# Kernel optimization log

Measured on AMD Instinct MI355X. Metric: run time of the kernel, lower is better.

Reference implementation:

```python
import jax, jax.numpy as jnp
import numpy as np

B, S = 256, 512
NQ = 1000           # n_skills
MEM, DK, DV, FC = 20, 50, 200, 50  # memory_size, key dim, value dim, final fc dim


def _kaiming(key, shape, fan_in):
    return jax.random.normal(key, shape) * np.float32(np.sqrt(2.0 / fan_in))


def setup_inputs() -> dict:
    key = jax.random.key(0)
    ks = jax.random.split(key, 12)
    q_data = jax.random.randint(ks[0], (B, S), 0, NQ + 1)
    qa_data = jax.random.randint(ks[1], (B, S), 0, 2 * NQ + 1)
    u = jax.random.uniform(ks[2], (B * S,))
    # target: -1 = masked/padding, else binary label (matches target.ge(0) masking)
    target = jnp.where(u < 0.1, -1.0, (u > 0.55).astype(jnp.float32))
    q_embed_w = _kaiming(ks[3], (NQ + 1, DK), DK)
    qa_embed_w = _kaiming(ks[4], (2 * NQ + 1, DV), DV)
    memory_key = _kaiming(ks[5], (MEM, DK), DK)
    init_memory_value = _kaiming(ks[6], (MEM, DV), DV)
    erase_w = _kaiming(ks[7], (DV, DV), DV)
    erase_b = jnp.zeros((DV,), jnp.float32)
    add_w = _kaiming(ks[8], (DV, DV), DV)
    add_b = jnp.zeros((DV,), jnp.float32)
    read_w = _kaiming(ks[9], (DV + FC, FC), DV + FC)
    read_b = jnp.zeros((FC,), jnp.float32)
    pred_w = _kaiming(ks[10], (FC, 1), FC)
    pred_b = jnp.zeros((1,), jnp.float32)
    return dict(q_data=q_data, qa_data=qa_data, target=target,
                q_embed_w=q_embed_w, qa_embed_w=qa_embed_w,
                memory_key=memory_key, init_memory_value=init_memory_value,
                erase_w=erase_w, erase_b=erase_b, add_w=add_w, add_b=add_b,
                read_w=read_w, read_b=read_b, pred_w=pred_w, pred_b=pred_b)


def reference(q_data, qa_data, target, q_embed_w, qa_embed_w, memory_key,
              init_memory_value, erase_w, erase_b, add_w, add_b,
              read_w, read_b, pred_w, pred_b):
    b = q_data.shape[0]
    q_e = q_embed_w[q_data]     # [B,S,DK]
    qa_e = qa_embed_w[qa_data]  # [B,S,DV]
    Mv0 = jnp.broadcast_to(init_memory_value, (b, MEM, DV))

    def step(Mv, xs):
        q_t, qa_t = xs                                        # [B,DK], [B,DV]
        corr = jax.nn.softmax(q_t @ memory_key.T, axis=1)     # [B,MEM] addressing
        read = jnp.einsum('bm,bmd->bd', corr, Mv)             # weighted read
        erase = jax.nn.sigmoid(qa_t @ erase_w + erase_b)      # [B,DV]
        add = jnp.tanh(qa_t @ add_w + add_b)                  # [B,DV]
        w = corr[:, :, None]                                  # [B,MEM,1]
        Mv = Mv * (1.0 - w * erase[:, None, :]) + w * add[:, None, :]
        return Mv, read

    _, reads = jax.lax.scan(step, Mv0, (q_e.transpose(1, 0, 2), qa_e.transpose(1, 0, 2)))
    reads = reads.transpose(1, 0, 2)                          # [B,S,DV]
    x = jnp.concatenate([reads, q_e], axis=-1)                # [B,S,DV+FC]
    h = jnp.tanh(x @ read_w + read_b)                         # [B,S,FC]
    logits = (h @ pred_w + pred_b).reshape(-1)                # [B*S]
    mask = target >= 0.0
    t = jnp.where(mask, target, 0.0)
    # numerically-stable BCE-with-logits, masked mean
    bce = jnp.maximum(logits, 0.0) - logits * t + jnp.log1p(jnp.exp(-jnp.abs(logits)))
    loss = jnp.sum(jnp.where(mask, bce, 0.0)) / jnp.maximum(mask.sum(), 1)
    return loss, jax.nn.sigmoid(logits)
```

## Files before the change

kernel.cpp:

```cpp
#include <hip/hip_runtime.h>
#include <math.h>

#define B_   256
#define S_   512
#define NQ_  1000
#define MEM_ 20
#define DK_  50
#define DV_  200
#define FC_  50
#define RPB  4
#define CHK  16
#define CLEN (S_/CHK)
#define NKS  7
#define XS_STRIDE 232
#define CORR_STRIDE 12
#define NB_EA    ((2*NQ_+1+RPB-1)/RPB)
#define NB_CORR  4
#define NB_WPACK 7
#define NB_HQ    251
#define PREP1_BLOCKS (NB_EA+NB_CORR)
#define MM_BLOCKS (B_*CHK)
#define SCANA_BLOCKS (B_*(CHK-1))
#define SCANA_TOTAL (SCANA_BLOCKS+NB_WPACK+NB_HQ)

typedef __attribute__((ext_vector_type(8))) short bf16x8_t;
typedef __attribute__((ext_vector_type(4))) float f32x4_t;
typedef __attribute__((ext_vector_type(2))) _Float16 f16x2_t;

static __device__ __forceinline__ f16x2_t h2(unsigned u){ return __builtin_bit_cast(f16x2_t, u); }
static __device__ __forceinline__ unsigned h2u(f16x2_t v){ return __builtin_bit_cast(unsigned, v); }
static __device__ __forceinline__ unsigned packh2(float x, float y){
  unsigned short bx = __builtin_bit_cast(unsigned short, (_Float16)x);
  unsigned short by = __builtin_bit_cast(unsigned short, (_Float16)y);
  return (unsigned)bx | ((unsigned)by << 16);
}
static __device__ __forceinline__ f16x2_t pkfma16(f16x2_t a, f16x2_t b, f16x2_t c){
  return __builtin_elementwise_fma(a, b, c);
}

static __device__ __forceinline__ unsigned short f2bf(float f){
  unsigned u = __float_as_uint(f);
  unsigned r = u + 0x7fffu + ((u >> 16) & 1u);
  return (unsigned short)(r >> 16);
}
static __device__ __forceinline__ float ftanh(float x){
  float e = __expf(2.f*x);
  return 1.f - 2.f*__builtin_amdgcn_rcpf(e+1.f);
}
static __device__ __forceinline__ float fsigm(float x){
  return __builtin_amdgcn_rcpf(1.f+__expf(-x));
}

__global__ __launch_bounds__(256) void k_prep1(
    const float* __restrict__ qaw,
    const float* __restrict__ ew, const float* __restrict__ eb,
    const float* __restrict__ aw, const float* __restrict__ ab,
    uint2* __restrict__ eaTab,
    const float* __restrict__ qw, const float* __restrict__ mk,
    unsigned* __restrict__ corrH){
  __shared__ float qa[RPB*DV_];
  int blk = blockIdx.x;
  if(blk < NB_EA){
    int row0 = blk*RPB;
    for(int i=threadIdx.x; i<RPB*DV_; i+=256){
      int r = i/DV_, cc = i - r*DV_;
      int row = row0 + r;
      qa[i] = (row <= 2*NQ_) ? qaw[row*DV_+cc] : 0.f;
    }
    __syncthreads();
    int d = threadIdx.x;
    if(d >= DV_) return;
    float accE[RPB], accA[RPB];
    #pragma unroll
    for(int r=0;r<RPB;++r){ accE[r] = eb[d]; accA[r] = ab[d]; }
    float we0 = ew[d], wa0 = aw[d];
    for(int j=0;j<DV_;++j){
      int jn = (j+1 < DV_) ? j+1 : j;
      float we1 = ew[jn*DV_+d];
      float wa1 = aw[jn*DV_+d];
      #pragma unroll
      for(int r=0;r<RPB;++r){
        float x = qa[r*DV_+j];
        accE[r] = fmaf(x, we0, accE[r]);
        accA[r] = fmaf(x, wa0, accA[r]);
      }
      we0 = we1; wa0 = wa1;
    }
    #pragma unroll
    for(int r=0;r<RPB;++r){
      int row = row0 + r;
      if(row <= 2*NQ_){
        unsigned he = (unsigned)__builtin_bit_cast(unsigned short, (_Float16)fsigm(accE[r]));
        unsigned ha = (unsigned)__builtin_bit_cast(unsigned short, (_Float16)ftanh(accA[r]));
        eaTab[(size_t)row*DV_+d] = make_uint2(he*0x10001u, ha*0x10001u);
      }
    }
  } else {
    int q = (blk-NB_EA)*256 + threadIdx.x;
    if(q > NQ_) return;
    float qv[DK_];
    #pragma unroll
    for(int j=0;j<DK_;++j) qv[j] = qw[q*DK_+j];
    float s[MEM_]; float mx = -1e30f;
    #pragma unroll
    for(int m=0;m<MEM_;++m){
      float acc = 0.f;
      #pragma unroll
      for(int j=0;j<DK_;++j) acc = fmaf(qv[j], mk[m*DK_+j], acc);
      s[m] = acc; mx = fmaxf(mx, acc);
    }
    float sum = 0.f;
    #pragma unroll
    for(int m=0;m<MEM_;++m){ s[m] = __expf(s[m]-mx); sum += s[m]; }
    float inv = __builtin_amdgcn_rcpf(sum);
    #pragma unroll
    for(int i=0;i<MEM_/2;++i)
      corrH[q*CORR_STRIDE+i] = packh2(s[2*i]*inv, s[2*i+1]*inv);
  }
}

__global__ __launch_bounds__(256,8) void k_scanA(const int* __restrict__ qd,
    const int* __restrict__ qad,
    const unsigned* __restrict__ corrH,
    const uint2* __restrict__ eaTab,
    unsigned* __restrict__ ABu,
    const float* __restrict__ qw,
    const float* __restrict__ rw, const float* __restrict__ rb,
    const float* __restrict__ pw,
    unsigned short* __restrict__ WpFrag, float* __restrict__ pwPad,
    float* __restrict__ hq){
  const int blk = blockIdx.x;
  if(blk >= SCANA_BLOCKS){
    int xblk = blk - SCANA_BLOCKS;
    if(xblk < NB_WPACK){
      int ks = xblk;
      int nt = threadIdx.x >> 6;
      int lane = threadIdx.x & 63;
      int quad = lane >> 4, col = lane & 15;
      int n = nt*16 + col;
      unsigned short tmp[8];
      #pragma unroll
      for(int j=0;j<8;++j){
        int k = ks*32 + quad*8 + j;
        tmp[j] = (k < DV_ && n < FC_) ? f2bf(rw[k*FC_+n]) : (unsigned short)0;
      }
      uint4* dst = reinterpret_cast<uint4*>(WpFrag + ((size_t)(ks*4+nt)*64 + lane)*8);
      *dst = *reinterpret_cast<const uint4*>(tmp);
      if(ks == 0 && threadIdx.x < 64)
        pwPad[threadIdx.x] = (threadIdx.x < FC_) ? pw[threadIdx.x] : 0.f;
    } else {
      int idx = (xblk-NB_WPACK)*256 + threadIdx.x;
      int q = idx >> 6, n = idx & 63;
      if(q > NQ_) return;
      float v = 0.f;
      if(n < FC_){
        float acc = rb[n];
        #pragma unroll
        for(int j=0;j<DK_;++j)
          acc = fmaf(qw[q*DK_+j], rw[(DV_+j)*FC_+n], acc);
        v = acc;
      }
      hq[q*64+n] = v;
    }
    return;
  }

  const int b = blk / (CHK-1), c = blk % (CHK-1);
  const int d = threadIdx.x;
  const int dc = (d < DV_) ? d : DV_-1;
  const bool act = (d < DV_);
  const int* __restrict__ qp  = qd  + b*S_ + c*CLEN;
  const int* __restrict__ qap = qad + b*S_ + c*CLEN;

  const f16x2_t one2h = {(_Float16)1.f, (_Float16)1.f};
  f16x2_t A2[MEM_/2], B2[MEM_/2];
  #pragma unroll
  for(int i=0;i<MEM_/2;++i){ A2[i] = one2h; B2[i] = (f16x2_t){(_Float16)0.f,(_Float16)0.f}; }

  int q2   = qp[1];
  int qaT2 = qap[2];
  int qaT3 = qap[3];
  int q1s  = __builtin_amdgcn_readfirstlane(qp[0]);
  const unsigned* cp0 = corrH + q1s*CORR_STRIDE;
  uint4 ca = *(const uint4*)(cp0);
  uint4 cb = *(const uint4*)(cp0+4);
  uint2 cc = *(const uint2*)(cp0+8);
  uint2 ea  = eaTab[(size_t)qap[0]*DV_ + dc];
  uint2 ean = eaTab[(size_t)qap[1]*DV_ + dc];

  #pragma unroll 4
  for(int t=0;t<CLEN;++t){
    int t2 = (t+2 < CLEN) ? t+2 : CLEN-1;
    int t4 = (t+4 < CLEN) ? t+4 : CLEN-1;
    int q3 = qp[t2];
    int qaN = qap[t4];
    int qs = __builtin_amdgcn_readfirstlane(q2);
    const unsigned* cpn_ = corrH + qs*CORR_STRIDE;
    uint4 na = *(const uint4*)(cpn_);
    uint4 nb = *(const uint4*)(cpn_+4);
    uint2 nc = *(const uint2*)(cpn_+8);
    uint2 eann = eaTab[(size_t)qaT2*DV_ + dc];

    const f16x2_t ee = h2(ea.x), aa = h2(ea.y);
    #define UPDA(u, i) { \
      f16x2_t cp = h2(u); \
      f16x2_t al = pkfma16(-cp, ee, one2h); \
      f16x2_t be = cp*aa; \
      A2[i] = A2[i]*al; \
      B2[i] = pkfma16(al, B2[i], be); }
    UPDA(ca.x, 0)  UPDA(ca.y, 1)  UPDA(ca.z, 2)  UPDA(ca.w, 3)
    UPDA(cb.x, 4)  UPDA(cb.y, 5)  UPDA(cb.z, 6)  UPDA(cb.w, 7)
    UPDA(cc.x, 8)  UPDA(cc.y, 9)
    #undef UPDA

    ca=na; cb=nb; cc=nc;
    ea=ean; ean=eann;
    q2=q3; qaT2=qaT3; qaT3=qaN;
  }
  if(act){
    unsigned* base = ABu + ((size_t)(b*(CHK-1) + c)*MEM_)*DV_ + d;
    #pragma unroll
    for(int i=0;i<MEM_/2;++i){
      unsigned a01 = h2u(A2[i]);
      unsigned b01 = h2u(B2[i]);
      base[(size_t)(2*i)*DV_]   = (a01 & 0xffffu) | (b01 << 16);
      base[(size_t)(2*i+1)*DV_] = (a01 >> 16)     | (b01 & 0xffff0000u);
    }
  }
}

__global__ __launch_bounds__(256) void k_prefix(const float* __restrict__ mv0,
    const unsigned* __restrict__ ABu, unsigned* __restrict__ Mv0p){
  int i = blockIdx.x*256 + threadIdx.x;
  if(i >= B_*(MEM_/2)*DV_) return;
  int d = i % DV_;
  int p = (i / DV_) % (MEM_/2);
  int b = i / (DV_*(MEM_/2));
  float MvE = mv0[(2*p)*DV_+d];
  float MvO = mv0[(2*p+1)*DV_+d];
  #pragma unroll
  for(int c=1;c<CHK;++c){
    unsigned vE = ABu[((size_t)(b*(CHK-1) + (c-1))*MEM_ + 2*p)*DV_ + d];
    unsigned vO = ABu[((size_t)(b*(CHK-1) + (c-1))*MEM_ + 2*p+1)*DV_ + d];
    MvE = fmaf((float)h2(vE)[0], MvE, (float)h2(vE)[1]);
    MvO = fmaf((float)h2(vO)[0], MvO, (float)h2(vO)[1]);
    Mv0p[((size_t)(b*CHK + c)*(MEM_/2) + p)*DV_ + d] = packh2(MvE, MvO);
  }
}

__global__ __launch_bounds__(256,8) void k_scan_mm(const int* __restrict__ qd,
    const int* __restrict__ qad,
    const unsigned* __restrict__ corrH,
    const uint2* __restrict__ eaTab,
    const float* __restrict__ mv0,
    const unsigned* __restrict__ Mv0p,
    const unsigned short* __restrict__ WpFrag,
    const float* __restrict__ hq,
    const float* __restrict__ pwPad, const float* __restrict__ pb,
    const float* __restrict__ target,
    float* __restrict__ out, float2* __restrict__ partials){
  __shared__ unsigned short Xs[CLEN*XS_STRIDE];
  __shared__ float sred[2][2][16];
  __shared__ float sbce[4];

  const int blk = blockIdx.x;
  const int b = blk >> 4, c = blk & (CHK-1);
  const int d = threadIdx.x;
  const int dc = (d < DV_) ? d : DV_-1;
  const bool act = (d < DV_);
  const bool padw = (d < 224);
  const int* __restrict__ qp  = qd  + b*S_ + c*CLEN;
  const int* __restrict__ qap = qad + b*S_ + c*CLEN;

  const int wave = threadIdx.x >> 6;
  const int lane = threadIdx.x & 63;
  const int col  = lane & 15, quad = lane >> 4;
  const int rt   = wave & 1;
  const int nh   = wave >> 1;
  const int mbase = rt*16;

  int qpre[4];
  #pragma unroll
  for(int reg=0;reg<4;++reg) qpre[reg] = qp[mbase + quad*4 + reg];

  f16x2_t Mv2[MEM_/2];
  if(c == 0){
    #pragma unroll
    for(int i=0;i<MEM_/2;++i)
      Mv2[i] = (f16x2_t){ (_Float16)mv0[(2*i)*DV_+dc], (_Float16)mv0[(2*i+1)*DV_+dc] };
  } else {
    const unsigned* base = Mv0p + ((size_t)(b*CHK + c)*(MEM_/2))*DV_ + dc;
    #pragma unroll
    for(int i=0;i<MEM_/2;++i)
      Mv2[i] = h2(base[(size_t)i*DV_]);
  }

  int q2   = qp[1];
  int qaT2 = qap[2];
  int qaT3 = qap[3];
  int q1s  = __builtin_amdgcn_readfirstlane(qp[0]);
  const unsigned* cp0 = corrH + q1s*CORR_STRIDE;
  uint4 ca = *(const uint4*)(cp0);
  uint4 cb = *(const uint4*)(cp0+4);
  uint2 cc = *(const uint2*)(cp0+8);
  uint2 ea  = eaTab[(size_t)qap[0]*DV_ + dc];
  uint2 ean = eaTab[(size_t)qap[1]*DV_ + dc];

  #pragma unroll 4
  for(int t=0;t<CLEN;++t){
    int t2 = (t+2 < CLEN) ? t+2 : CLEN-1;
    int t4 = (t+4 < CLEN) ? t+4 : CLEN-1;
    int q3 = qp[t2];
    int qaN = qap[t4];
    int qs = __builtin_amdgcn_readfirstlane(q2);
    const unsigned* cpn_ = corrH + qs*CORR_STRIDE;
    uint4 na = *(const uint4*)(cpn_);
    uint4 nb = *(const uint4*)(cpn_+4);
    uint2 nc = *(const uint2*)(cpn_+8);
    uint2 eann = eaTab[(size_t)qaT2*DV_ + dc];

    const f16x2_t ee = h2(ea.x), aa = h2(ea.y);
    float rd0 = 0.f, rd1 = 0.f;
    #define UPD2(u, i, acc) { \
      f16x2_t cp = h2(u); \
      acc = __builtin_amdgcn_fdot2(cp, Mv2[i], acc, false); \
      f16x2_t tt = pkfma16(-Mv2[i], ee, aa); \
      Mv2[i] = pkfma16(cp, tt, Mv2[i]); }
    UPD2(ca.x, 0, rd0)  UPD2(ca.y, 1, rd1)  UPD2(ca.z, 2, rd0)  UPD2(ca.w, 3, rd1)
    UPD2(cb.x, 4, rd0)  UPD2(cb.y, 5, rd1)  UPD2(cb.z, 6, rd0)  UPD2(cb.w, 7, rd1)
    UPD2(cc.x, 8, rd0)  UPD2(cc.y, 9, rd1)
    #undef UPD2

    if(padw) Xs[t*XS_STRIDE + d] = act ? f2bf(rd0+rd1) : (unsigned short)0;

    ca=na; cb=nb; cc=nc;
    ea=ean; ean=eann;
    q2=q3; qaT2=qaT3; qaT3=qaN;
  }
  __syncthreads();

  float hqv[4][2];
  #pragma unroll
  for(int reg=0;reg<4;++reg)
    #pragma unroll
    for(int j=0;j<2;++j)
      hqv[reg][j] = hq[qpre[reg]*64 + (nh*2+j)*16 + col];

  f32x4_t acc[2];
  acc[0] = (f32x4_t){0.f,0.f,0.f,0.f};
  acc[1] = (f32x4_t){0.f,0.f,0.f,0.f};

  #pragma unroll
  for(int ks=0;ks<NKS;++ks){
    bf16x8_t a = *reinterpret_cast<const bf16x8_t*>(Xs + (mbase+col)*XS_STRIDE + quad*8 + ks*32);
    #pragma unroll
    for(int j=0;j<2;++j){
      int nt = nh*2 + j;
      bf16x8_t bfr = *reinterpret_cast<const bf16x8_t*>(WpFrag + ((size_t)(ks*4+nt)*64 + lane)*8);
      acc[j] = __builtin_amdgcn_mfma_f32_16x16x32_bf16(a, bfr, acc[j], 0, 0, 0);
    }
  }

  float part[4];
  #pragma unroll
  for(int reg=0;reg<4;++reg){
    float s = 0.f;
    #pragma unroll
    for(int j=0;j<2;++j){
      int n = (nh*2+j)*16 + col;
      float h = acc[j][reg] + hqv[reg][j];
      s = fmaf(pwPad[n], ftanh(h), s);
    }
    part[reg] = s;
  }
  #pragma unroll
  for(int off=1; off<16; off<<=1){
    #pragma unroll
    for(int reg=0;reg<4;++reg) part[reg] += __shfl_xor(part[reg], off, 64);
  }
  if(col == 0){
    #pragma unroll
    for(int reg=0;reg<4;++reg) sred[rt][nh][quad*4+reg] = part[reg];
  }
  __syncthreads();

  float bce = 0.f, cnt = 0.f;
  if(nh == 0 && col == 0){
    float pbv = pb[0];
    #pragma unroll
    for(int reg=0;reg<4;++reg){
      int idx = quad*4 + reg;
      int mloc = mbase + idx;
      int row = b*S_ + c*CLEN + mloc;
      float logit = sred[rt][0][idx] + sred[rt][1][idx] + pbv;
      out[1+row] = fsigm(logit);
      float t = target[row];
      if(t >= 0.f){
        cnt += 1.f;
        bce += fmaxf(logit,0.f) - logit*t + log1pf(__expf(-fabsf(logit)));
      }
    }
  }
  bce += __shfl_xor(bce, 16, 64); cnt += __shfl_xor(cnt, 16, 64);
  bce += __shfl_xor(bce, 32, 64); cnt += __shfl_xor(cnt, 32, 64);
  if(lane == 0 && nh == 0){ sbce[wave] = bce; sbce[2+wave] = cnt; }
  __syncthreads();
  if(threadIdx.x == 0)
    partials[blk] = make_float2(sbce[0]+sbce[1], sbce[2]+sbce[3]);
}

__global__ __launch_bounds__(256) void k_fin(const float2* __restrict__ partials,
                                             float* __restrict__ out){
  float bce = 0.f, cnt = 0.f;
  for(int i=threadIdx.x; i<MM_BLOCKS; i+=256){
    float2 p = partials[i];
    bce += p.x; cnt += p.y;
  }
  #pragma unroll
  for(int off=32; off>0; off>>=1){
    bce += __shfl_down(bce, off, 64);
    cnt += __shfl_down(cnt, off, 64);
  }
  __shared__ float sb[4], sc[4];
  int w = threadIdx.x >> 6;
  if((threadIdx.x & 63) == 0){ sb[w] = bce; sc[w] = cnt; }
  __syncthreads();
  if(threadIdx.x == 0){
    float Bt = sb[0]+sb[1]+sb[2]+sb[3];
    float Ct = sc[0]+sc[1]+sc[2]+sc[3];
    out[0] = Bt / fmaxf(Ct, 1.f);
  }
}

extern "C" void kernel_launch(void* const* d_in, const int* in_sizes, int n_in,
                              void* d_out, int out_size, void* d_ws, size_t ws_size,
                              hipStream_t stream){
  const int*   qd     = (const int*)d_in[0];
  const int*   qad    = (const int*)d_in[1];
  const float* target = (const float*)d_in[2];
  const float* qw     = (const float*)d_in[3];
  const float* qaw    = (const float*)d_in[4];
  const float* mk     = (const float*)d_in[5];
  const float* mv0    = (const float*)d_in[6];
  const float* ew     = (const float*)d_in[7];
  const float* eb     = (const float*)d_in[8];
  const float* aw     = (const float*)d_in[9];
  const float* ab     = (const float*)d_in[10];
  const float* rw     = (const float*)d_in[11];
  const float* rb     = (const float*)d_in[12];
  const float* pw     = (const float*)d_in[13];
  const float* pb     = (const float*)d_in[14];
  float* out = (float*)d_out;

  char* ws = (char*)d_ws;
  size_t off = 0;
  float2* partials = (float2*)(ws + off);            off += (size_t)MM_BLOCKS*8;
  unsigned* corrH = (unsigned*)(ws + off);           off += (((size_t)(NQ_+1)*CORR_STRIDE*4 + 255)/256)*256;
  uint2* eaTab    = (uint2*)(ws + off);              off += (((size_t)(2*NQ_+1)*DV_*8 + 255)/256)*256;
  unsigned* ABu   = (unsigned*)(ws + off);           off += (size_t)SCANA_BLOCKS*MEM_*DV_*4;
  unsigned* Mv0p  = (unsigned*)(ws + off);           off += (size_t)MM_BLOCKS*(MEM_/2)*DV_*4;
  unsigned short* WpFrag = (unsigned short*)(ws + off); off += ((size_t)NKS*4*64*8*2 + 255)/256*256;
  float* pwPad    = (float*)(ws + off);              off += 256;
  float* hq       = (float*)(ws + off);              off += (size_t)(NQ_+1)*64*4;

  k_prep1<<<dim3(PREP1_BLOCKS), dim3(256), 0, stream>>>(qaw, ew, eb, aw, ab, eaTab,
                                                        qw, mk, corrH);
  k_scanA<<<dim3(SCANA_TOTAL), dim3(256), 0, stream>>>(qd, qad, corrH, eaTab,
                                                       ABu, qw, rw, rb, pw, WpFrag, pwPad, hq);
  k_prefix<<<dim3((B_*(MEM_/2)*DV_+255)/256), dim3(256), 0, stream>>>(mv0, ABu, Mv0p);
  k_scan_mm<<<dim3(MM_BLOCKS), dim3(256), 0, stream>>>(qd, qad, corrH, eaTab,
                                                       mv0, Mv0p, WpFrag, hq, pwPad, pb, target, out, partials);
  k_fin<<<dim3(1), dim3(256), 0, stream>>>(partials, out);
}
```

Baseline: 225.8 us.

## Pack erase/add table into one word and deepen scan prefetch pipeline

The erase/add lookup table now stores one packed half2 word per entry (erase low, add high) instead of two pre-splatted half2 words, halving the table size and the per-step gather bytes. The scan loops splat the halves in registers and prefetch addressing weights two steps ahead and erase/add entries three steps ahead, to better hide gather latency in both scan kernels. The cost is extra shuffle instructions per step and more live registers, which could pressure occupancy under the launch bound of 8 blocks.

Result: no change. 222.1 us (-1.6%).

```diff
diff --git a/kernel.cpp b/kernel.cpp
--- a/kernel.cpp
+++ b/kernel.cpp
@@ -37,6 +37,8 @@
 static __device__ __forceinline__ f16x2_t pkfma16(f16x2_t a, f16x2_t b, f16x2_t c){
   return __builtin_elementwise_fma(a, b, c);
 }
+static __device__ __forceinline__ f16x2_t splat_l(f16x2_t p){ return __builtin_shufflevector(p, p, 0, 0); }
+static __device__ __forceinline__ f16x2_t splat_h(f16x2_t p){ return __builtin_shufflevector(p, p, 1, 1); }
 
 static __device__ __forceinline__ unsigned short f2bf(float f){
   unsigned u = __float_as_uint(f);
@@ -55,7 +57,7 @@
     const float* __restrict__ qaw,
     const float* __restrict__ ew, const float* __restrict__ eb,
     const float* __restrict__ aw, const float* __restrict__ ab,
-    uint2* __restrict__ eaTab,
+    unsigned* __restrict__ eaTab,
     const float* __restrict__ qw, const float* __restrict__ mk,
     unsigned* __restrict__ corrH){
   __shared__ float qa[RPB*DV_];
@@ -92,7 +94,7 @@
       if(row <= 2*NQ_){
         unsigned he = (unsigned)__builtin_bit_cast(unsigned short, (_Float16)fsigm(accE[r]));
         unsigned ha = (unsigned)__builtin_bit_cast(unsigned short, (_Float16)ftanh(accA[r]));
-        eaTab[(size_t)row*DV_+d] = make_uint2(he*0x10001u, ha*0x10001u);
+        eaTab[(size_t)row*DV_+d] = he | (ha << 16);
       }
     }
   } else {
@@ -122,7 +124,7 @@
 __global__ __launch_bounds__(256,8) void k_scanA(const int* __restrict__ qd,
     const int* __restrict__ qad,
     const unsigned* __restrict__ corrH,
-    const uint2* __restrict__ eaTab,
+    const unsigned* __restrict__ eaTab,
     unsigned* __restrict__ ABu,
     const float* __restrict__ qw,
     const float* __restrict__ rw, const float* __restrict__ rb,
@@ -177,45 +179,49 @@
   #pragma unroll
   for(int i=0;i<MEM_/2;++i){ A2[i] = one2h; B2[i] = (f16x2_t){(_Float16)0.f,(_Float16)0.f}; }
 
-  int q2   = qp[1];
-  int qaT2 = qap[2];
-  int qaT3 = qap[3];
-  int q1s  = __builtin_amdgcn_readfirstlane(qp[0]);
-  const unsigned* cp0 = corrH + q1s*CORR_STRIDE;
-  uint4 ca = *(const uint4*)(cp0);
-  uint4 cb = *(const uint4*)(cp0+4);
-  uint2 cc = *(const uint2*)(cp0+8);
-  uint2 ea  = eaTab[(size_t)qap[0]*DV_ + dc];
-  uint2 ean = eaTab[(size_t)qap[1]*DV_ + dc];
+  unsigned ea0 = eaTab[(size_t)qap[0]*DV_ + dc];
+  unsigned ea1 = eaTab[(size_t)qap[1]*DV_ + dc];
+  unsigned ea2 = eaTab[(size_t)qap[2]*DV_ + dc];
+  int qa3 = qap[3], qa4 = qap[4], qa5 = qap[5];
+  int s0 = __builtin_amdgcn_readfirstlane(qp[0]);
+  int s1 = __builtin_amdgcn_readfirstlane(qp[1]);
+  const unsigned* c0p = corrH + s0*CORR_STRIDE;
+  uint4 ca0 = *(const uint4*)(c0p); uint4 cb0 = *(const uint4*)(c0p+4); uint2 cc0 = *(const uint2*)(c0p+8);
+  const unsigned* c1p = corrH + s1*CORR_STRIDE;
+  uint4 ca1 = *(const uint4*)(c1p); uint4 cb1 = *(const uint4*)(c1p+4); uint2 cc1 = *(const uint2*)(c1p+8);
+  int qn2 = qp[2], qn3 = qp[3];
 
   #pragma unroll 4
   for(int t=0;t<CLEN;++t){
-    int t2 = (t+2 < CLEN) ? t+2 : CLEN-1;
+    int qs = __builtin_amdgcn_readfirstlane(qn2);
+    const unsigned* cnp = corrH + qs*CORR_STRIDE;
+    uint4 ca2 = *(const uint4*)(cnp);
+    uint4 cb2 = *(const uint4*)(cnp+4);
+    uint2 cc2 = *(const uint2*)(cnp+8);
+    unsigned eanew = eaTab[(size_t)qa3*DV_ + dc];
     int t4 = (t+4 < CLEN) ? t+4 : CLEN-1;
-    int q3 = qp[t2];
-    int qaN = qap[t4];
-    int qs = __builtin_amdgcn_readfirstlane(q2);
-    const unsigned* cpn_ = corrH + qs*CORR_STRIDE;
-    uint4 na = *(const uint4*)(cpn_);
-    uint4 nb = *(const uint4*)(cpn_+4);
-    uint2 nc = *(const uint2*)(cpn_+8);
-    uint2 eann = eaTab[(size_t)qaT2*DV_ + dc];
-
-    const f16x2_t ee = h2(ea.x), aa = h2(ea.y);
+    int qnew = qp[t4];
+    int t6 = (t+6 < CLEN) ? t+6 : CLEN-1;
+    int qanew = qap[t6];
+
+    f16x2_t pe = h2(ea0);
+    const f16x2_t ee = splat_l(pe), aa = splat_h(pe);
     #define UPDA(u, i) { \
       f16x2_t cp = h2(u); \
       f16x2_t al = pkfma16(-cp, ee, one2h); \
       f16x2_t be = cp*aa; \
       A2[i] = A2[i]*al; \
       B2[i] = pkfma16(al, B2[i], be); }
-    UPDA(ca.x, 0)  UPDA(ca.y, 1)  UPDA(ca.z, 2)  UPDA(ca.w, 3)
-    UPDA(cb.x, 4)  UPDA(cb.y, 5)  UPDA(cb.z, 6)  UPDA(cb.w, 7)
-    UPDA(cc.x, 8)  UPDA(cc.y, 9)
+    UPDA(ca0.x, 0)  UPDA(ca0.y, 1)  UPDA(ca0.z, 2)  UPDA(ca0.w, 3)
+    UPDA(cb0.x, 4)  UPDA(cb0.y, 5)  UPDA(cb0.z, 6)  UPDA(cb0.w, 7)
+    UPDA(cc0.x, 8)  UPDA(cc0.y, 9)
     #undef UPDA
 
-    ca=na; cb=nb; cc=nc;
-    ea=ean; ean=eann;
-    q2=q3; qaT2=qaT3; qaT3=qaN;
+    ca0=ca1; cb0=cb1; cc0=cc1;
+    ca1=ca2; cb1=cb2; cc1=cc2;
+    qn2=qn3; qn3=qnew;
+    ea0=ea1; ea1=ea2; ea2=eanew;
+    qa3=qa4; qa4=qa5; qa5=qanew;
   }
   if(act){
     unsigned* base = ABu + ((size_t)(b*(CHK-1) + c)*MEM_)*DV_ + d;
@@ -251,7 +257,7 @@
 __global__ __launch_bounds__(256,8) void k_scan_mm(const int* __restrict__ qd,
     const int* __restrict__ qad,
     const unsigned* __restrict__ corrH,
-    const uint2* __restrict__ eaTab,
+    const unsigned* __restrict__ eaTab,
     const float* __restrict__ mv0,
     const unsigned* __restrict__ Mv0p,
     const unsigned short* __restrict__ WpFrag,
@@ -295,47 +301,51 @@
       Mv2[i] = h2(base[(size_t)i*DV_]);
   }
 
-  int q2   = qp[1];
-  int qaT2 = qap[2];
-  int qaT3 = qap[3];
-  int q1s  = __builtin_amdgcn_readfirstlane(qp[0]);
-  const unsigned* cp0 = corrH + q1s*CORR_STRIDE;
-  uint4 ca = *(const uint4*)(cp0);
-  uint4 cb = *(const uint4*)(cp0+4);
-  uint2 cc = *(const uint2*)(cp0+8);
-  uint2 ea  = eaTab[(size_t)qap[0]*DV_ + dc];
-  uint2 ean = eaTab[(size_t)qap[1]*DV_ + dc];
+  unsigned ea0 = eaTab[(size_t)qap[0]*DV_ + dc];
+  unsigned ea1 = eaTab[(size_t)qap[1]*DV_ + dc];
+  unsigned ea2 = eaTab[(size_t)qap[2]*DV_ + dc];
+  int qa3 = qap[3], qa4 = qap[4], qa5 = qap[5];
+  int s0 = __builtin_amdgcn_readfirstlane(qp[0]);
+  int s1 = __builtin_amdgcn_readfirstlane(qp[1]);
+  const unsigned* c0p = corrH + s0*CORR_STRIDE;
+  uint4 ca0 = *(const uint4*)(c0p); uint4 cb0 = *(const uint4*)(c0p+4); uint2 cc0 = *(const uint2*)(c0p+8);
+  const unsigned* c1p = corrH + s1*CORR_STRIDE;
+  uint4 ca1 = *(const uint4*)(c1p); uint4 cb1 = *(const uint4*)(c1p+4); uint2 cc1 = *(const uint2*)(c1p+8);
+  int qn2 = qp[2], qn3 = qp[3];
 
   #pragma unroll 4
   for(int t=0;t<CLEN;++t){
-    int t2 = (t+2 < CLEN) ? t+2 : CLEN-1;
+    int qs = __builtin_amdgcn_readfirstlane(qn2);
+    const unsigned* cnp = corrH + qs*CORR_STRIDE;
+    uint4 ca2 = *(const uint4*)(cnp);
+    uint4 cb2 = *(const uint4*)(cnp+4);
+    uint2 cc2 = *(const uint2*)(cnp+8);
+    unsigned eanew = eaTab[(size_t)qa3*DV_ + dc];
     int t4 = (t+4 < CLEN) ? t+4 : CLEN-1;
-    int q3 = qp[t2];
-    int qaN = qap[t4];
-    int qs = __builtin_amdgcn_readfirstlane(q2);
-    const unsigned* cpn_ = corrH + qs*CORR_STRIDE;
-    uint4 na = *(const uint4*)(cpn_);
-    uint4 nb = *(const uint4*)(cpn_+4);
-    uint2 nc = *(const uint2*)(cpn_+8);
-    uint2 eann = eaTab[(size_t)qaT2*DV_ + dc];
-
-    const f16x2_t ee = h2(ea.x), aa = h2(ea.y);
+    int qnew = qp[t4];
+    int t6 = (t+6 < CLEN) ? t+6 : CLEN-1;
+    int qanew = qap[t6];
+
+    f16x2_t pe = h2(ea0);
+    const f16x2_t ee = splat_l(pe), aa = splat_h(pe);
     float rd0 = 0.f, rd1 = 0.f;
     #define UPD2(u, i, acc) { \
       f16x2_t cp = h2(u); \
       acc = __builtin_amdgcn_fdot2(cp, Mv2[i], acc, false); \
       f16x2_t tt = pkfma16(-Mv2[i], ee, aa); \
       Mv2[i] = pkfma16(cp, tt, Mv2[i]); }
-    UPD2(ca.x, 0, rd0)  UPD2(ca.y, 1, rd1)  UPD2(ca.z, 2, rd0)  UPD2(ca.w, 3, rd1)
-    UPD2(cb.x, 4, rd0)  UPD2(cb.y, 5, rd1)  UPD2(cb.z, 6, rd0)  UPD2(cb.w, 7, rd1)
-    UPD2(cc.x, 8, rd0)  UPD2(cc.y, 9, rd1)
+    UPD2(ca0.x, 0, rd0)  UPD2(ca0.y, 1, rd1)  UPD2(ca0.z, 2, rd0)  UPD2(ca0.w, 3, rd1)
+    UPD2(cb0.x, 4, rd0)  UPD2(cb0.y, 5, rd1)  UPD2(cb0.z, 6, rd0)  UPD2(cb0.w, 7, rd1)
+    UPD2(cc0.x, 8, rd0)  UPD2(cc0.y, 9, rd1)
     #undef UPD2
 
     if(padw) Xs[t*XS_STRIDE + d] = act ? f2bf(rd0+rd1) : (unsigned short)0;
 
-    ca=na; cb=nb; cc=nc;
-    ea=ean; ean=eann;
-    q2=q3; qaT2=qaT3; qaT3=qaN;
+    ca0=ca1; cb0=cb1; cc0=cc1;
+    ca1=ca2; cb1=cb2; cc1=cc2;
+    qn2=qn3; qn3=qnew;
+    ea0=ea1; ea1=ea2; ea2=eanew;
+    qa3=qa4; qa4=qa5; qa5=qanew;
   }
   __syncthreads();
 
@@ -456,7 +466,7 @@
   size_t off = 0;
   float2* partials = (float2*)(ws + off);            off += (size_t)MM_BLOCKS*8;
   unsigned* corrH = (unsigned*)(ws + off);           off += (((size_t)(NQ_+1)*CORR_STRIDE*4 + 255)/256)*256;
-  uint2* eaTab    = (uint2*)(ws + off);              off += (((size_t)(2*NQ_+1)*DV_*8 + 255)/256)*256;
+  unsigned* eaTab = (unsigned*)(ws + off);           off += (((size_t)(2*NQ_+1)*DV_*4 + 255)/256)*256;
   unsigned* ABu   = (unsigned*)(ws + off);           off += (size_t)SCANA_BLOCKS*MEM_*DV_*4;
   unsigned* Mv0p  = (unsigned*)(ws + off);           off += (size_t)MM_BLOCKS*(MEM_/2)*DV_*4;
   unsigned short* WpFrag = (unsigned short*)(ws + off); off += ((size_t)NKS*4*64*8*2 + 255)/256*256;
```

## Replace chunked parallel scan with one sequential fp32 scan block per batch row

Applied to the files above, without the earlier changes.

Removes the chunk-parallel scan (scanA, prefix, per-chunk scan+matmul) and has one 256-thread block per batch row walk all 512 steps sequentially in fp32. Memory state stays in packed fp32 registers, and the read projection with MFMA and the BCE run after each 32-step chunk inside the same block. Precomputed tables switch from fp16 to fp32, and the prep work is merged into a single kernel. This drops two kernel launches and the intermediate A/B and prefix buffers. The cost is that only 256 blocks run, leaving most of the GPU idle, with a long serial dependency chain per block.

Result: slower. 243.8 us (+8.0%).

```diff
diff --git a/kernel.cpp b/kernel.cpp
--- a/kernel.cpp
+++ b/kernel.cpp
@@ -13,31 +13,20 @@
 #define CLEN (S_/CHK)
 #define NKS  7
 #define XS_STRIDE 232
-#define CORR_STRIDE 12
+#define CORRF_STRIDE 24
 #define NB_EA    ((2*NQ_+1+RPB-1)/RPB)
 #define NB_CORR  4
 #define NB_WPACK 7
 #define NB_HQ    251
-#define PREP1_BLOCKS (NB_EA+NB_CORR)
-#define MM_BLOCKS (B_*CHK)
-#define SCANA_BLOCKS (B_*(CHK-1))
-#define SCANA_TOTAL (SCANA_BLOCKS+NB_WPACK+NB_HQ)
+#define PREP_BLOCKS (NB_EA+NB_CORR+NB_WPACK+NB_HQ)
 
 typedef __attribute__((ext_vector_type(8))) short bf16x8_t;
 typedef __attribute__((ext_vector_type(4))) float f32x4_t;
-typedef __attribute__((ext_vector_type(2))) _Float16 f16x2_t;
-
-static __device__ __forceinline__ f16x2_t h2(unsigned u){ return __builtin_bit_cast(f16x2_t, u); }
-static __device__ __forceinline__ unsigned h2u(f16x2_t v){ return __builtin_bit_cast(unsigned, v); }
-static __device__ __forceinline__ unsigned packh2(float x, float y){
-  unsigned short bx = __builtin_bit_cast(unsigned short, (_Float16)x);
-  unsigned short by = __builtin_bit_cast(unsigned short, (_Float16)y);
-  return (unsigned)bx | ((unsigned)by << 16);
-}
-static __device__ __forceinline__ f16x2_t pkfma16(f16x2_t a, f16x2_t b, f16x2_t c){
+typedef __attribute__((ext_vector_type(2))) float f32x2_t;
+
+static __device__ __forceinline__ f32x2_t pkfma32(f32x2_t a, f32x2_t b, f32x2_t c){
   return __builtin_elementwise_fma(a, b, c);
 }
-
 static __device__ __forceinline__ unsigned short f2bf(float f){
   unsigned u = __float_as_uint(f);
   unsigned r = u + 0x7fffu + ((u >> 16) & 1u);
@@ -51,13 +40,21 @@
   return __builtin_amdgcn_rcpf(1.f+__expf(-x));
 }
 
+#define RFL(x) __builtin_amdgcn_readfirstlane(x)
+
+struct corr20 { float4 v0, v1, v2, v3, v4; };
+
 __global__ __launch_bounds__(256) void k_prep1(
     const float* __restrict__ qaw,
     const float* __restrict__ ew, const float* __restrict__ eb,
     const float* __restrict__ aw, const float* __restrict__ ab,
-    uint2* __restrict__ eaTab,
+    float2* __restrict__ eaTabF,
     const float* __restrict__ qw, const float* __restrict__ mk,
-    unsigned* __restrict__ corrH){
+    float* __restrict__ corrF,
+    const float* __restrict__ rw, const float* __restrict__ rb,
+    const float* __restrict__ pw,
+    unsigned short* __restrict__ WpFrag, float* __restrict__ pwPad,
+    float* __restrict__ hq){
   __shared__ float qa[RPB*DV_];
   int blk = blockIdx.x;
   if(blk < NB_EA){
@@ -89,13 +86,10 @@
     #pragma unroll
     for(int r=0;r<RPB;++r){
       int row = row0 + r;
-      if(row <= 2*NQ_){
-        unsigned he = (unsigned)__builtin_bit_cast(unsigned short, (_Float16)fsigm(accE[r]));
-        unsigned ha = (unsigned)__builtin_bit_cast(unsigned short, (_Float16)ftanh(accA[r]));
-        eaTab[(size_t)row*DV_+d] = make_uint2(he*0x10001u, ha*0x10001u);
-      }
-    }
-  } else {
+      if(row <= 2*NQ_)
+        eaTabF[(size_t)row*DV_+d] = make_float2(fsigm(accE[r]), ftanh(accA[r]));
+    }
+  } else if(blk < NB_EA+NB_CORR){
     int q = (blk-NB_EA)*256 + threadIdx.x;
     if(q > NQ_) return;
     float qv[DK_];
@@ -114,146 +108,44 @@
     for(int m=0;m<MEM_;++m){ s[m] = __expf(s[m]-mx); sum += s[m]; }
     float inv = __builtin_amdgcn_rcpf(sum);
     #pragma unroll
-    for(int i=0;i<MEM_/2;++i)
-      corrH[q*CORR_STRIDE+i] = packh2(s[2*i]*inv, s[2*i+1]*inv);
+    for(int m=0;m<MEM_;++m) corrF[q*CORRF_STRIDE+m] = s[m]*inv;
+  } else if(blk < NB_EA+NB_CORR+NB_WPACK){
+    int ks = blk - (NB_EA+NB_CORR);
+    int nt = threadIdx.x >> 6;
+    int lane = threadIdx.x & 63;
+    int quad = lane >> 4, col = lane & 15;
+    int n = nt*16 + col;
+    unsigned short tmp[8];
+    #pragma unroll
+    for(int j=0;j<8;++j){
+      int k = ks*32 + quad*8 + j;
+      tmp[j] = (k < DV_ && n < FC_) ? f2bf(rw[k*FC_+n]) : (unsigned short)0;
+    }
+    uint4* dst = reinterpret_cast<uint4*>(WpFrag + ((size_t)(ks*4+nt)*64 + lane)*8);
+    *dst = *reinterpret_cast<const uint4*>(tmp);
+    if(ks == 0 && threadIdx.x < 64)
+      pwPad[threadIdx.x] = (threadIdx.x < FC_) ? pw[threadIdx.x] : 0.f;
+  } else {
+    int idx = (blk-(NB_EA+NB_CORR+NB_WPACK))*256 + threadIdx.x;
+    int q = idx >> 6, n = idx & 63;
+    if(q > NQ_) return;
+    float v = 0.f;
+    if(n < FC_){
+      float acc = rb[n];
+      #pragma unroll
+      for(int j=0;j<DK_;++j)
+        acc = fmaf(qw[q*DK_+j], rw[(DV_+j)*FC_+n], acc);
+      v = acc;
+    }
+    hq[q*64+n] = v;
   }
 }
 
-__global__ __launch_bounds__(256,8) void k_scanA(const int* __restrict__ qd,
+__global__ __launch_bounds__(256,1) void k_seq(const int* __restrict__ qd,
     const int* __restrict__ qad,
-    const unsigned* __restrict__ corrH,
-    const uint2* __restrict__ eaTab,
-    unsigned* __restrict__ ABu,
-    const float* __restrict__ qw,
-    const float* __restrict__ rw, const float* __restrict__ rb,
-    const float* __restrict__ pw,
-    unsigned short* __restrict__ WpFrag, float* __restrict__ pwPad,
-    float* __restrict__ hq){
-  const int blk = blockIdx.x;
-  if(blk >= SCANA_BLOCKS){
-    int xblk = blk - SCANA_BLOCKS;
-    if(xblk < NB_WPACK){
-      int ks = xblk;
-      int nt = threadIdx.x >> 6;
-      int lane = threadIdx.x & 63;
-      int quad = lane >> 4, col = lane & 15;
-      int n = nt*16 + col;
-      unsigned short tmp[8];
-      #pragma unroll
-      for(int j=0;j<8;++j){
-        int k = ks*32 + quad*8 + j;
-        tmp[j] = (k < DV_ && n < FC_) ? f2bf(rw[k*FC_+n]) : (unsigned short)0;
-      }
-      uint4* dst = reinterpret_cast<uint4*>(WpFrag + ((size_t)(ks*4+nt)*64 + lane)*8);
-      *dst = *reinterpret_cast<const uint4*>(tmp);
-      if(ks == 0 && threadIdx.x < 64)
-        pwPad[threadIdx.x] = (threadIdx.x < FC_) ? pw[threadIdx.x] : 0.f;
-    } else {
-      int idx = (xblk-NB_WPACK)*256 + threadIdx.x;
-      int q = idx >> 6, n = idx & 63;
-      if(q > NQ_) return;
-      float v = 0.f;
-      if(n < FC_){
-        float acc = rb[n];
-        #pragma unroll
-        for(int j=0;j<DK_;++j)
-          acc = fmaf(qw[q*DK_+j], rw[(DV_+j)*FC_+n], acc);
-        v = acc;
-      }
-      hq[q*64+n] = v;
-    }
-    return;
-  }
-
-  const int b = blk / (CHK-1), c = blk % (CHK-1);
-  const int d = threadIdx.x;
-  const int dc = (d < DV_) ? d : DV_-1;
-  const bool act = (d < DV_);
-  const int* __restrict__ qp  = qd  + b*S_ + c*CLEN;
-  const int* __restrict__ qap = qad + b*S_ + c*CLEN;
-
-  const f16x2_t one2h = {(_Float16)1.f, (_Float16)1.f};
-  f16x2_t A2[MEM_/2], B2[MEM_/2];
-  #pragma unroll
-  for(int i=0;i<MEM_/2;++i){ A2[i] = one2h; B2[i] = (f16x2_t){(_Float16)0.f,(_Float16)0.f}; }
-
-  int q2   = qp[1];
-  int qaT2 = qap[2];
-  int qaT3 = qap[3];
-  int q1s  = __builtin_amdgcn_readfirstlane(qp[0]);
-  const unsigned* cp0 = corrH + q1s*CORR_STRIDE;
-  uint4 ca = *(const uint4*)(cp0);
-  uint4 cb = *(const uint4*)(cp0+4);
-  uint2 cc = *(const uint2*)(cp0+8);
-  uint2 ea  = eaTab[(size_t)qap[0]*DV_ + dc];
-  uint2 ean = eaTab[(size_t)qap[1]*DV_ + dc];
-
-  #pragma unroll 4
-  for(int t=0;t<CLEN;++t){
-    int t2 = (t+2 < CLEN) ? t+2 : CLEN-1;
-    int t4 = (t+4 < CLEN) ? t+4 : CLEN-1;
-    int q3 = qp[t2];
-    int qaN = qap[t4];
-    int qs = __builtin_amdgcn_readfirstlane(q2);
-    const unsigned* cpn_ = corrH + qs*CORR_STRIDE;
-    uint4 na = *(const uint4*)(cpn_);
-    uint4 nb = *(const uint4*)(cpn_+4);
-    uint2 nc = *(const uint2*)(cpn_+8);
-    uint2 eann = eaTab[(size_t)qaT2*DV_ + dc];
-
-    const f16x2_t ee = h2(ea.x), aa = h2(ea.y);
-    #define UPDA(u, i) { \
-      f16x2_t cp = h2(u); \
-      f16x2_t al = pkfma16(-cp, ee, one2h); \
-      f16x2_t be = cp*aa; \
-      A2[i] = A2[i]*al; \
-      B2[i] = pkfma16(al, B2[i], be); }
-    UPDA(ca.x, 0)  UPDA(ca.y, 1)  UPDA(ca.z, 2)  UPDA(ca.w, 3)
-    UPDA(cb.x, 4)  UPDA(cb.y, 5)  UPDA(cb.z, 6)  UPDA(cb.w, 7)
-    UPDA(cc.x, 8)  UPDA(cc.y, 9)
-    #undef UPDA
-
-    ca=na; cb=nb; cc=nc;
-    ea=ean; ean=eann;
-    q2=q3; qaT2=qaT3; qaT3=qaN;
-  }
-  if(act){
-    unsigned* base = ABu + ((size_t)(b*(CHK-1) + c)*MEM_)*DV_ + d;
-    #pragma unroll
-    for(int i=0;i<MEM_/2;++i){
-      unsigned a01 = h2u(A2[i]);
-      unsigned b01 = h2u(B2[i]);
-      base[(size_t)(2*i)*DV_]   = (a01 & 0xffffu) | (b01 << 16);
-      base[(size_t)(2*i+1)*DV_] = (a01 >> 16)     | (b01 & 0xffff0000u);
-    }
-  }
-}
-
-__global__ __launch_bounds__(256) void k_prefix(const float* __restrict__ mv0,
-    const unsigned* __restrict__ ABu, unsigned* __restrict__ Mv0p){
-  int i = blockIdx.x*256 + threadIdx.x;
-  if(i >= B_*(MEM_/2)*DV_) return;
-  int d = i % DV_;
-  int p = (i / DV_) % (MEM_/2);
-  int b = i / (DV_*(MEM_/2));
-  float MvE = mv0[(2*p)*DV_+d];
-  float MvO = mv0[(2*p+1)*DV_+d];
-  #pragma unroll
-  for(int c=1;c<CHK;++c){
-    unsigned vE = ABu[((size_t)(b*(CHK-1) + (c-1))*MEM_ + 2*p)*DV_ + d];
-    unsigned vO = ABu[((size_t)(b*(CHK-1) + (c-1))*MEM_ + 2*p+1)*DV_ + d];
-    MvE = fmaf((float)h2(vE)[0], MvE, (float)h2(vE)[1]);
-    MvO = fmaf((float)h2(vO)[0], MvO, (float)h2(vO)[1]);
-    Mv0p[((size_t)(b*CHK + c)*(MEM_/2) + p)*DV_ + d] = packh2(MvE, MvO);
-  }
-}
-
-__global__ __launch_bounds__(256,8) void k_scan_mm(const int* __restrict__ qd,
-    const int* __restrict__ qad,
-    const unsigned* __restrict__ corrH,
-    const uint2* __restrict__ eaTab,
+    const float* __restrict__ corrF,
+    const float2* __restrict__ eaTabF,
     const float* __restrict__ mv0,
-    const unsigned* __restrict__ Mv0p,
     const unsigned short* __restrict__ WpFrag,
     const float* __restrict__ hq,
     const float* __restrict__ pwPad, const float* __restrict__ pb,
@@ -263,14 +155,13 @@
   __shared__ float sred[2][2][16];
   __shared__ float sbce[4];
 
-  const int blk = blockIdx.x;
-  const int b = blk >> 4, c = blk & (CHK-1);
+  const int b = blockIdx.x;
   const int d = threadIdx.x;
   const int dc = (d < DV_) ? d : DV_-1;
   const bool act = (d < DV_);
   const bool padw = (d < 224);
-  const int* __restrict__ qp  = qd  + b*S_ + c*CLEN;
-  const int* __restrict__ qap = qad + b*S_ + c*CLEN;
+  const int* __restrict__ qp  = qd  + b*S_;
+  const int* __restrict__ qap = qad + b*S_;
 
   const int wave = threadIdx.x >> 6;
   const int lane = threadIdx.x & 63;
@@ -279,143 +170,151 @@
   const int nh   = wave >> 1;
   const int mbase = rt*16;
 
-  int qpre[4];
+  f32x2_t Mv[MEM_/2];
   #pragma unroll
-  for(int reg=0;reg<4;++reg) qpre[reg] = qp[mbase + quad*4 + reg];
-
-  f16x2_t Mv2[MEM_/2];
-  if(c == 0){
-    #pragma unroll
-    for(int i=0;i<MEM_/2;++i)
-      Mv2[i] = (f16x2_t){ (_Float16)mv0[(2*i)*DV_+dc], (_Float16)mv0[(2*i+1)*DV_+dc] };
-  } else {
-    const unsigned* base = Mv0p + ((size_t)(b*CHK + c)*(MEM_/2))*DV_ + dc;
-    #pragma unroll
-    for(int i=0;i<MEM_/2;++i)
-      Mv2[i] = h2(base[(size_t)i*DV_]);
+  for(int i=0;i<MEM_/2;++i)
+    Mv[i] = (f32x2_t){ mv0[(2*i)*DV_+dc], mv0[(2*i+1)*DV_+dc] };
+
+  #define LD_EAF(DST, ROW) { int _r = RFL(ROW); DST = eaTabF[(size_t)_r*DV_ + dc]; }
+  #define LD_CORRF(CS, QV) { const float4* _p = (const float4*)(corrF + (size_t)(QV)*CORRF_STRIDE); \
+    CS.v0=_p[0]; CS.v1=_p[1]; CS.v2=_p[2]; CS.v3=_p[3]; CS.v4=_p[4]; }
+
+  float2 ea0, ea1, ea2, ea3;
+  LD_EAF(ea0, qap[0])  LD_EAF(ea1, qap[1])  LD_EAF(ea2, qap[2])  LD_EAF(ea3, qap[3])
+  corr20 cs0, cs1, cs2, cs3;
+  { int t0=qp[0], t1=qp[1], t2=qp[2], t3=qp[3];
+    LD_CORRF(cs0, t0) LD_CORRF(cs1, t1) LD_CORRF(cs2, t2) LD_CORRF(cs3, t3) }
+  int qa_i0=qap[4], qa_i1=qap[5], qa_i2=qap[6], qa_i3=qap[7];
+  int qv_i0=qp[4],  qv_i1=qp[5],  qv_i2=qp[6],  qv_i3=qp[7];
+
+  int qpreC[4];
+  #pragma unroll
+  for(int reg=0;reg<4;++reg) qpreC[reg] = qp[mbase + quad*4 + reg];
+  float pwv[2];
+  #pragma unroll
+  for(int j=0;j<2;++j) pwv[j] = pwPad[(nh*2+j)*16 + col];
+  const float pbv = pb[0];
+
+  float bceAcc = 0.f, cntAcc = 0.f;
+
+  #define PAIR(CPX, CPY, i) { \
+    f32x2_t cp = {CPX, CPY}; \
+    racc = pkfma32(cp, Mv[i], racc); \
+    f32x2_t tt_ = pkfma32(-Mv[i], ee, aa); \
+    Mv[i] = pkfma32(cp, tt_, Mv[i]); }
+  #define STEP(TT_, EA, CS) { \
+    f32x2_t ee = {EA.x, EA.x}, aa = {EA.y, EA.y}; \
+    f32x2_t racc = {0.f, 0.f}; \
+    PAIR(CS.v0.x, CS.v0.y, 0) PAIR(CS.v0.z, CS.v0.w, 1) \
+    PAIR(CS.v1.x, CS.v1.y, 2) PAIR(CS.v1.z, CS.v1.w, 3) \
+    PAIR(CS.v2.x, CS.v2.y, 4) PAIR(CS.v2.z, CS.v2.w, 5) \
+    PAIR(CS.v3.x, CS.v3.y, 6) PAIR(CS.v3.z, CS.v3.w, 7) \
+    PAIR(CS.v4.x, CS.v4.y, 8) PAIR(CS.v4.z, CS.v4.w, 9) \
+    float rd = racc[0] + racc[1]; \
+    if(padw) Xs[(TT_)*XS_STRIDE + d] = act ? f2bf(rd) : (unsigned short)0; }
+  #define SLOT(K, EAr, CSr, QAr, QVr) { \
+    STEP(tt+(K), EAr, CSr) \
+    LD_EAF(EAr, QAr) \
+    LD_CORRF(CSr, QVr) \
+    { int g8 = c*CLEN + tt + (K) + 8; int ix = (g8 < S_) ? g8 : S_-1; \
+      QAr = qap[ix]; QVr = qp[ix]; } }
+
+  #pragma unroll 1
+  for(int c=0;c<CHK;++c){
+    int qpreN[4];
+    { int cn = (c+1 < CHK) ? c+1 : c;
+      #pragma unroll
+      for(int reg=0;reg<4;++reg) qpreN[reg] = qp[cn*CLEN + mbase + quad*4 + reg]; }
+
+    #pragma unroll 1
+    for(int tt=0; tt<CLEN; tt+=4){
+      SLOT(0, ea0, cs0, qa_i0, qv_i0)
+      SLOT(1, ea1, cs1, qa_i1, qv_i1)
+      SLOT(2, ea2, cs2, qa_i2, qv_i2)
+      SLOT(3, ea3, cs3, qa_i3, qv_i3)
+    }
+
+    float hqv[4][2];
+    #pragma unroll
+    for(int reg=0;reg<4;++reg)
+      #pragma unroll
+      for(int j=0;j<2;++j)
+        hqv[reg][j] = hq[qpreC[reg]*64 + (nh*2+j)*16 + col];
+
+    __syncthreads();
+
+    f32x4_t acc[2];
+    acc[0] = (f32x4_t){0.f,0.f,0.f,0.f};
+    acc[1] = (f32x4_t){0.f,0.f,0.f,0.f};
+    #pragma unroll
+    for(int ks=0;ks<NKS;++ks){
+      bf16x8_t a = *reinterpret_cast<const bf16x8_t*>(Xs + (mbase+col)*XS_STRIDE + quad*8 + ks*32);
+      #pragma unroll
+      for(int j=0;j<2;++j){
+        int nt = nh*2 + j;
+        bf16x8_t bfr = *reinterpret_cast<const bf16x8_t*>(WpFrag + ((size_t)(ks*4+nt)*64 + lane)*8);
+        acc[j] = __builtin_amdgcn_mfma_f32_16x16x32_bf16(a, bfr, acc[j], 0, 0, 0);
+      }
+    }
+
+    float part[4];
+    #pragma unroll
+    for(int reg=0;reg<4;++reg){
+      float s = 0.f;
+      #pragma unroll
+      for(int j=0;j<2;++j){
+        float h = acc[j][reg] + hqv[reg][j];
+        s = fmaf(pwv[j], ftanh(h), s);
+      }
+      part[reg] = s;
+    }
+    #pragma unroll
+    for(int off=1; off<16; off<<=1){
+      #pragma unroll
+      for(int reg=0;reg<4;++reg) part[reg] += __shfl_xor(part[reg], off, 64);
+    }
+    if(col == 0){
+      #pragma unroll
+      for(int reg=0;reg<4;++reg) sred[rt][nh][quad*4+reg] = part[reg];
+    }
+    __syncthreads();
+
+    if(nh == 0 && col == 0){
+      #pragma unroll
+      for(int reg=0;reg<4;++reg){
+        int idx = quad*4 + reg;
+        int mloc = mbase + idx;
+        int row = b*S_ + c*CLEN + mloc;
+        float logit = sred[rt][0][idx] + sred[rt][1][idx] + pbv;
+        out[1+row] = fsigm(logit);
+        float t = target[row];
+        if(t >= 0.f){
+          cntAcc += 1.f;
+          bceAcc += fmaxf(logit,0.f) - logit*t + log1pf(__expf(-fabsf(logit)));
+        }
+      }
+    }
+    #pragma unroll
+    for(int reg=0;reg<4;++reg) qpreC[reg] = qpreN[reg];
   }
-
-  int q2   = qp[1];
-  int qaT2 = qap[2];
-  int qaT3 = qap[3];
-  int q1s  = __builtin_amdgcn_readfirstlane(qp[0]);
-  const unsigned* cp0 = corrH + q1s*CORR_STRIDE;
-  uint4 ca = *(const uint4*)(cp0);
-  uint4 cb = *(const uint4*)(cp0+4);
-  uint2 cc = *(const uint2*)(cp0+8);
-  uint2 ea  = eaTab[(size_t)qap[0]*DV_ + dc];
-  uint2 ean = eaTab[(size_t)qap[1]*DV_ + dc];
-
-  #pragma unroll 4
-  for(int t=0;t<CLEN;++t){
-    int t2 = (t+2 < CLEN) ? t+2 : CLEN-1;
-    int t4 = (t+4 < CLEN) ? t+4 : CLEN-1;
-    int q3 = qp[t2];
-    int qaN = qap[t4];
-    int qs = __builtin_amdgcn_readfirstlane(q2);
-    const unsigned* cpn_ = corrH + qs*CORR_STRIDE;
-    uint4 na = *(const uint4*)(cpn_);
-    uint4 nb = *(const uint4*)(cpn_+4);
-    uint2 nc = *(const uint2*)(cpn_+8);
-    uint2 eann = eaTab[(size_t)qaT2*DV_ + dc];
-
-    const f16x2_t ee = h2(ea.x), aa = h2(ea.y);
-    float rd0 = 0.f, rd1 = 0.f;
-    #define UPD2(u, i, acc) { \
-      f16x2_t cp = h2(u); \
-      acc = __builtin_amdgcn_fdot2(cp, Mv2[i], acc, false); \
-      f16x2_t tt = pkfma16(-Mv2[i], ee, aa); \
-      Mv2[i] = pkfma16(cp, tt, Mv2[i]); }
-    UPD2(ca.x, 0, rd0)  UPD2(ca.y, 1, rd1)  UPD2(ca.z, 2, rd0)  UPD2(ca.w, 3, rd1)
-    UPD2(cb.x, 4, rd0)  UPD2(cb.y, 5, rd1)  UPD2(cb.z, 6, rd0)  UPD2(cb.w, 7, rd1)
-    UPD2(cc.x, 8, rd0)  UPD2(cc.y, 9, rd1)
-    #undef UPD2
-
-    if(padw) Xs[t*XS_STRIDE + d] = act ? f2bf(rd0+rd1) : (unsigned short)0;
-
-    ca=na; cb=nb; cc=nc;
-    ea=ean; ean=eann;
-    q2=q3; qaT2=qaT3; qaT3=qaN;
-  }
-  __syncthreads();
-
-  float hqv[4][2];
-  #pragma unroll
-  for(int reg=0;reg<4;++reg)
-    #pragma unroll
-    for(int j=0;j<2;++j)
-      hqv[reg][j] = hq[qpre[reg]*64 + (nh*2+j)*16 + col];
-
-  f32x4_t acc[2];
-  acc[0] = (f32x4_t){0.f,0.f,0.f,0.f};
-  acc[1] = (f32x4_t){0.f,0.f,0.f,0.f};
-
-  #pragma unroll
-  for(int ks=0;ks<NKS;++ks){
-    bf16x8_t a = *reinterpret_cast<const bf16x8_t*>(Xs + (mbase+col)*XS_STRIDE + quad*8 + ks*32);
-    #pragma unroll
-    for(int j=0;j<2;++j){
-      int nt = nh*2 + j;
-      bf16x8_t bfr = *reinterpret_cast<const bf16x8_t*>(WpFrag + ((size_t)(ks*4+nt)*64 + lane)*8);
-      acc[j] = __builtin_amdgcn_mfma_f32_16x16x32_bf16(a, bfr, acc[j], 0, 0, 0);
-    }
-  }
-
-  float part[4];
-  #pragma unroll
-  for(int reg=0;reg<4;++reg){
-    float s = 0.f;
-    #pragma unroll
-    for(int j=0;j<2;++j){
-      int n = (nh*2+j)*16 + col;
-      float h = acc[j][reg] + hqv[reg][j];
-      s = fmaf(pwPad[n], ftanh(h), s);
-    }
-    part[reg] = s;
-  }
-  #pragma unroll
-  for(int off=1; off<16; off<<=1){
-    #pragma unroll
-    for(int reg=0;reg<4;++reg) part[reg] += __shfl_xor(part[reg], off, 64);
-  }
-  if(col == 0){
-    #pragma unroll
-    for(int reg=0;reg<4;++reg) sred[rt][nh][quad*4+reg] = part[reg];
-  }
-  __syncthreads();
-
-  float bce = 0.f, cnt = 0.f;
-  if(nh == 0 && col == 0){
-    float pbv = pb[0];
-    #pragma unroll
-    for(int reg=0;reg<4;++reg){
-      int idx = quad*4 + reg;
-      int mloc = mbase + idx;
-      int row = b*S_ + c*CLEN + mloc;
-      float logit = sred[rt][0][idx] + sred[rt][1][idx] + pbv;
-      out[1+row] = fsigm(logit);
-      float t = target[row];
-      if(t >= 0.f){
-        cnt += 1.f;
-        bce += fmaxf(logit,0.f) - logit*t + log1pf(__expf(-fabsf(logit)));
-      }
-    }
-  }
-  bce += __shfl_xor(bce, 16, 64); cnt += __shfl_xor(cnt, 16, 64);
-  bce += __shfl_xor(bce, 32, 64); cnt += __shfl_xor(cnt, 32, 64);
-  if(lane == 0 && nh == 0){ sbce[wave] = bce; sbce[2+wave] = cnt; }
+  #undef SLOT
+  #undef STEP
+  #undef PAIR
+  #undef LD_CORRF
+  #undef LD_EAF
+
+  bceAcc += __shfl_xor(bceAcc, 16, 64); cntAcc += __shfl_xor(cntAcc, 16, 64);
+  bceAcc += __shfl_xor(bceAcc, 32, 64); cntAcc += __shfl_xor(cntAcc, 32, 64);
+  if(lane == 0 && nh == 0){ sbce[wave] = bceAcc; sbce[2+wave] = cntAcc; }
   __syncthreads();
   if(threadIdx.x == 0)
-    partials[blk] = make_float2(sbce[0]+sbce[1], sbce[2]+sbce[3]);
+    partials[b] = make_float2(sbce[0]+sbce[1], sbce[2]+sbce[3]);
 }
 
 __global__ __launch_bounds__(256) void k_fin(const float2* __restrict__ partials,
                                              float* __restrict__ out){
-  float bce = 0.f, cnt = 0.f;
-  for(int i=threadIdx.x; i<MM_BLOCKS; i+=256){
-    float2 p = partials[i];
-    bce += p.x; cnt += p.y;
-  }
+  float2 p = partials[threadIdx.x];
+  float bce = p.x, cnt = p.y;
   #pragma unroll
   for(int off=32; off>0; off>>=1){
     bce += __shfl_down(bce, off, 64);
@@ -454,21 +353,17 @@
 
   char* ws = (char*)d_ws;
   size_t off = 0;
-  float2* partials = (float2*)(ws + off);            off += (size_t)MM_BLOCKS*8;
-  unsigned* corrH = (unsigned*)(ws + off);           off += (((size_t)(NQ_+1)*CORR_STRIDE*4 + 255)/256)*256;
-  uint2* eaTab    = (uint2*)(ws + off);              off += (((size_t)(2*NQ_+1)*DV_*8 + 255)/256)*256;
-  unsigned* ABu   = (unsigned*)(ws + off);           off += (size_t)SCANA_BLOCKS*MEM_*DV_*4;
-  unsigned* Mv0p  = (unsigned*)(ws + off);           off += (size_t)MM_BLOCKS*(MEM_/2)*DV_*4;
+  float2* partials = (float2*)(ws + off);            off += (((size_t)B_*8 + 255)/256)*256;
+  float* corrF    = (float*)(ws + off);              off += (((size_t)(NQ_+1)*CORRF_STRIDE*4 + 255)/256)*256;
+  float2* eaTabF  = (float2*)(ws + off);             off += (((size_t)(2*NQ_+1)*DV_*8 + 255)/256)*256;
   unsigned short* WpFrag = (unsigned short*)(ws + off); off += ((size_t)NKS*4*64*8*2 + 255)/256*256;
   float* pwPad    = (float*)(ws + off);              off += 256;
   float* hq       = (float*)(ws + off);              off += (size_t)(NQ_+1)*64*4;
 
-  k_prep1<<<dim3(PREP1_BLOCKS), dim3(256), 0, stream>>>(qaw, ew, eb, aw, ab, eaTab,
-                                                        qw, mk, corrH);
-  k_scanA<<<dim3(SCANA_TOTAL), dim3(256), 0, stream>>>(qd, qad, corrH, eaTab,
-                                                       ABu, qw, rw, rb, pw, WpFrag, pwPad, hq);
-  k_prefix<<<dim3((B_*(MEM_/2)*DV_+255)/256), dim3(256), 0, stream>>>(mv0, ABu, Mv0p);
-  k_scan_mm<<<dim3(MM_BLOCKS), dim3(256), 0, stream>>>(qd, qad, corrH, eaTab,
-                                                       mv0, Mv0p, WpFrag, hq, pwPad, pb, target, out, partials);
+  k_prep1<<<dim3(PREP_BLOCKS), dim3(256), 0, stream>>>(qaw, ew, eb, aw, ab, eaTabF,
+                                                       qw, mk, corrF,
+                                                       rw, rb, pw, WpFrag, pwPad, hq);
+  k_seq<<<dim3(B_), dim3(256), 0, stream>>>(qd, qad, corrF, eaTabF, mv0,
+                                            WpFrag, hq, pwPad, pb, target, out, partials);
   k_fin<<<dim3(1), dim3(256), 0, stream>>>(partials, out);
 }
```
